# Optimization experiments

Measured on AMD Instinct MI355X. Metric: run time of the kernel, lower is better.

Reference implementation:

```python
import jax, jax.numpy as jnp
import numpy as np

N_GRAPHS = 500
CHAIN = 200
D_STATE = 64
HID = 128
NEG_SLOPE = 0.2  # PyG GATConv default


def setup_inputs() -> dict:
    key = jax.random.key(0)
    ks = jax.random.split(key, 9)
    N = N_GRAPHS * CHAIN
    # batched bidirectional chain graphs (as in create_chain_graph_batch)
    off = np.arange(N_GRAPHS, dtype=np.int32) * CHAIN
    a = (off[:, None] + np.arange(CHAIN - 1, dtype=np.int32)[None, :]).ravel()
    b = a + 1
    edge_index = jnp.asarray(np.stack([np.concatenate([a, b]), np.concatenate([b, a])]), dtype=jnp.int32)
    x = jax.random.normal(ks[0], (N, D_STATE), jnp.float32)
    s1 = 1.0 / np.sqrt(D_STATE)
    W1 = jax.random.normal(ks[1], (D_STATE, 2 * HID), jnp.float32) * s1
    att_src1 = jax.random.normal(ks[2], (2, HID), jnp.float32) * (1.0 / np.sqrt(HID))
    att_dst1 = jax.random.normal(ks[3], (2, HID), jnp.float32) * (1.0 / np.sqrt(HID))
    b1 = jnp.zeros((2 * HID,), jnp.float32)
    s2 = 1.0 / np.sqrt(2 * HID)
    W2 = jax.random.normal(ks[4], (2 * HID, HID), jnp.float32) * s2
    att_src2 = jax.random.normal(ks[5], (1, HID), jnp.float32) * (1.0 / np.sqrt(HID))
    att_dst2 = jax.random.normal(ks[6], (1, HID), jnp.float32) * (1.0 / np.sqrt(HID))
    b2 = jnp.zeros((HID,), jnp.float32)
    return {"x": x, "edge_index": edge_index, "W1": W1, "att_src1": att_src1,
            "att_dst1": att_dst1, "b1": b1, "W2": W2, "att_src2": att_src2,
            "att_dst2": att_dst2, "b2": b2}


def gat_conv(x, src, dst, W, att_src, att_dst, bias, concat):
    # PyG GATConv: per-head linear, additive attention, segment softmax over dst
    N = x.shape[0]
    H, C = att_src.shape
    h = (x @ W).reshape(N, H, C)                          # [N,H,C]
    a_s = (h * att_src).sum(-1)                           # [N,H]
    a_d = (h * att_dst).sum(-1)                           # [N,H]
    logits = jax.nn.leaky_relu(a_s[src] + a_d[dst], NEG_SLOPE)  # [E,H]
    m = jax.ops.segment_max(logits, dst, num_segments=N)
    e = jnp.exp(logits - m[dst])
    s = jax.ops.segment_sum(e, dst, num_segments=N)
    alpha = e / (s[dst] + 1e-16)                          # [E,H]
    out = jax.ops.segment_sum(h[src] * alpha[:, :, None], dst, num_segments=N)  # [N,H,C]
    out = out.reshape(N, H * C) if concat else out.mean(axis=1)
    return out + bias


def reference(x, edge_index, W1, att_src1, att_dst1, b1, W2, att_src2, att_dst2, b2):
    N = x.shape[0]
    loop = jnp.arange(N, dtype=edge_index.dtype)
    src = jnp.concatenate([edge_index[0], loop])  # add_self_loops=True (PyG default)
    dst = jnp.concatenate([edge_index[1], loop])
    h = gat_conv(x, src, dst, W1, att_src1, att_dst1, b1, concat=True)
    h = jax.nn.gelu(h, approximate=False)  # torch F.gelu default = exact erf
    h = gat_conv(h, src, dst, W2, att_src2, att_dst2, b2, concat=False)
    return jax.nn.gelu(h, approximate=False)
```

## Files before the change

kernel.cpp:

```cpp
#include <hip/hip_runtime.h>
#include <hip/hip_bf16.h>

#define NG 500
#define CH 200
#define NN (NG*CH)
#define DS 64
#define HDIM 128
#define C1 256
#define NEG_SLOPE 0.2f
#define GB 1563

typedef unsigned short ushort_t;
typedef __attribute__((ext_vector_type(8))) short bf16x8;
typedef __attribute__((ext_vector_type(4))) float f32x4;

__device__ __forceinline__ float us2f(ushort_t u){
  union { unsigned int i; float f; } v; v.i = ((unsigned int)u) << 16; return v.f;
}
__device__ __forceinline__ ushort_t f2us(float f){
  union { float f; unsigned int i; } v; v.f = f;
  unsigned int x = v.i;
  return (ushort_t)((x + 0x7fffu + ((x >> 16) & 1u)) >> 16);
}
__device__ __forceinline__ float lrelu(float v){ return v > 0.f ? v : NEG_SLOPE * v; }
__device__ __forceinline__ float gelu_fast(float x){
  float xc = fminf(fmaxf(x, -8.f), 8.f);
  float u  = 0.7978845608f * (xc + 0.044715f * xc * xc * xc);
  float e  = __expf(2.f * u);
  float t  = 1.f - 2.f / (e + 1.f);
  return 0.5f * x * (1.f + t);
}

__global__ void probe_dtype(const void* __restrict__ x, int* __restrict__ flag){
  __shared__ int cnt;
  if (threadIdx.x == 0) cnt = 0;
  __syncthreads();
  const ushort_t* p = (const ushort_t*)x;
  int local = 0;
  for (int i = threadIdx.x; i < 8192; i += 256) {
    float v = us2f(p[i]);
    if (!(fabsf(v) < 100.f)) local++;
  }
  atomicAdd(&cnt, local);
  __syncthreads();
  if (threadIdx.x == 0) flag[0] = (cnt > 16) ? 1 : 0;
}

__global__ void prep_w(const int* __restrict__ flag,
                       const void* W1, const void* as1, const void* ad1, const void* b1,
                       const void* W2, const void* as2, const void* ad2, const void* b2,
                       ushort_t* w1t, ushort_t* w2t,
                       float* asrc1f, float* adst1f, float* b1f,
                       float* asrc2f, float* adst2f, float* b2f)
{
  const bool F = flag[0] != 0;
  int i = blockIdx.x * 256 + threadIdx.x;
  #define LD(p, j) (F ? ((const float*)(p))[j] : us2f(((const ushort_t*)(p))[j]))
  if (i < 16384)      { int k = i >> 8, n = i & 255; w1t[n*64  + k] = f2us(LD(W1, i)); }
  else if (i < 49152) { int j = i - 16384, k = j >> 7, n = j & 127; w2t[n*256 + k] = f2us(LD(W2, j)); }
  else if (i < 49408) { asrc1f[i-49152] = LD(as1, i-49152); }
  else if (i < 49664) { adst1f[i-49408] = LD(ad1, i-49408); }
  else if (i < 49920) { b1f[i-49664]    = LD(b1,  i-49664); }
  else if (i < 50048) { asrc2f[i-49920] = LD(as2, i-49920); }
  else if (i < 50176) { adst2f[i-50048] = LD(ad2, i-50048); }
  else if (i < 50304) { b2f[i-50176]    = LD(b2,  i-50176); }
  #undef LD
}

__global__ __launch_bounds__(256, 3) void fused(
    const int* __restrict__ flag, const void* __restrict__ x,
    const ushort_t* __restrict__ w1t, const ushort_t* __restrict__ w2t,
    const float* __restrict__ asrc1f, const float* __restrict__ adst1f, const float* __restrict__ b1f,
    const float* __restrict__ asrc2f, const float* __restrict__ adst2f, const float* __restrict__ b2f,
    void* __restrict__ out)
{
  __shared__ ushort_t lds[22560];
  __shared__ float part_s[4][68], part_d[4][68];
  __shared__ float alp[66*8];
  ushort_t* As  = lds;
  ushort_t* Bs  = lds + 80*72;
  ushort_t* g1L = lds;
  ushort_t* Bs2 = lds + 68*264;

  const int t  = threadIdx.x;
  const int m0 = blockIdx.x * 64;
  const int l = t & 63, w = t >> 6;
  const int ln = l & 15, quad = l >> 4;
  const bool F = flag[0] != 0;

  #pragma unroll
  for (int i = 0; i < 5; i++) {
    int q = t + i*256;
    int r = q >> 4, off = (q & 15) * 4;
    int gr = m0 - 2 + r;
    ushort4 v = {0,0,0,0};
    if (r < 68 && gr >= 0 && gr < NN) {
      if (F) {
        float4 xv = *(const float4*)(&((const float*)x)[(size_t)gr*DS + off]);
        v.x = f2us(xv.x); v.y = f2us(xv.y); v.z = f2us(xv.z); v.w = f2us(xv.w);
      } else {
        v = *(const ushort4*)(&((const ushort_t*)x)[(size_t)gr*DS + off]);
      }
    }
    *(ushort4*)(&As[r*72 + off]) = v;
  }

  f32x4 acc[5][4];
  #pragma unroll
  for (int mi = 0; mi < 5; mi++)
    #pragma unroll
    for (int nj = 0; nj < 4; nj++) acc[mi][nj] = (f32x4){0.f,0.f,0.f,0.f};

  #pragma unroll
  for (int h = 0; h < 2; h++) {
    #pragma unroll
    for (int i = 0; i < 4; i++) {
      int u = t + i*256;
      int rl = u >> 3, off = (u & 7) * 8;
      int wv = rl >> 5, rem = rl & 31;
      int grow = wv*64 + h*32 + rem;
      *(uint4*)(&Bs[rl*72 + off]) = *(const uint4*)(&w1t[grow*64 + off]);
    }
    __syncthreads();
    #pragma unroll
    for (int ks = 0; ks < 2; ks++) {
      const int kk = ks*32 + quad*8;
      bf16x8 a[5], b[2];
      #pragma unroll
      for (int mi = 0; mi < 5; mi++) a[mi] = *(const bf16x8*)(&As[(mi*16 + ln)*72 + kk]);
      #pragma unroll
      for (int njl = 0; njl < 2; njl++) b[njl] = *(const bf16x8*)(&Bs[(w*32 + njl*16 + ln)*72 + kk]);
      #pragma unroll
      for (int mi = 0; mi < 5; mi++)
        #pragma unroll
        for (int njl = 0; njl < 2; njl++)
          acc[mi][2*h+njl] = __builtin_amdgcn_mfma_f32_16x16x32_bf16(a[mi], b[njl], acc[mi][2*h+njl], 0, 0, 0);
    }
    __syncthreads();
  }

  {
    float wsv[4], wdv[4];
    #pragma unroll
    for (int nj = 0; nj < 4; nj++) {
      wsv[nj] = asrc1f[w*64 + nj*16 + ln];
      wdv[nj] = adst1f[w*64 + nj*16 + ln];
    }
    #pragma unroll
    for (int mi = 0; mi < 5; mi++)
      #pragma unroll
      for (int r = 0; r < 4; r++) {
        float s = 0.f, d = 0.f;
        #pragma unroll
        for (int nj = 0; nj < 4; nj++) { s += acc[mi][nj][r] * wsv[nj]; d += acc[mi][nj][r] * wdv[nj]; }
        #pragma unroll
        for (int o = 1; o < 16; o <<= 1) { s += __shfl_xor(s, o, 64); d += __shfl_xor(d, o, 64); }
        int row = mi*16 + quad*4 + r;
        if (ln == 0 && row < 68) { part_s[w][row] = s; part_d[w][row] = d; }
      }
  }
  __syncthreads();

  if (t < 132) {
    int hh = (t >= 66) ? 1 : 0;
    int n  = t - 66*hh;
    int gj = m0 - 1 + n;
    int p  = gj % CH;
    float ad   = part_d[2*hh][n+1] + part_d[2*hh+1][n+1];
    float as_s = part_s[2*hh][n+1] + part_s[2*hh+1][n+1];
    float as_l = part_s[2*hh][n  ] + part_s[2*hh+1][n  ];
    float as_r = part_s[2*hh][n+2] + part_s[2*hh+1][n+2];
    bool hl = p > 0, hr = p < CH-1;
    float zs = lrelu(as_s + ad);
    float zl = hl ? lrelu(as_l + ad) : -1e30f;
    float zr = hr ? lrelu(as_r + ad) : -1e30f;
    float mx = fmaxf(zs, fmaxf(zl, zr));
    float el = hl ? __expf(zl - mx) : 0.f;
    float es = __expf(zs - mx);
    float er = hr ? __expf(zr - mx) : 0.f;
    float inv = 1.f / (el + es + er + 1e-16f);
    alp[n*8 + hh*4 + 0] = el*inv; alp[n*8 + hh*4 + 1] = es*inv; alp[n*8 + hh*4 + 2] = er*inv;
  }
  __syncthreads();

  {
    float b1v[4];
    #pragma unroll
    for (int nj = 0; nj < 4; nj++) b1v[nj] = b1f[w*64 + nj*16 + ln];
    if (t < 132) {
      int rr = (t < 66) ? 0 : 67;
      int c4 = ((t < 66) ? t : t - 66) * 4;
      ushort4 z = {0,0,0,0};
      *(ushort4*)(&g1L[rr*264 + c4]) = z;
    }
    const int head = w >> 1;
    #pragma unroll
    for (int mi = 0; mi < 5; mi++) {
      const int mip = (mi < 4) ? mi+1 : 4;
      const int mim = (mi > 0) ? mi-1 : 0;
      float hp3[4], hm0[4];
      #pragma unroll
      for (int nj = 0; nj < 4; nj++) {
        float up_a = __shfl(acc[mi ][nj][0], (l+16)&63, 64);
        float up_b = __shfl(acc[mip][nj][0], (l+16)&63, 64);
        float dn_a = __shfl(acc[mi ][nj][3], (l-16)&63, 64);
        float dn_b = __shfl(acc[mim][nj][3], (l-16)&63, 64);
        hp3[nj] = (quad < 3) ? up_a : up_b;
        hm0[nj] = (quad > 0) ? dn_a : dn_b;
      }
      #pragma unroll
      for (int r = 0; r < 4; r++) {
        int row = mi*16 + quad*4 + r;
        if (row >= 1 && row <= 66) {
          float4 av = *(const float4*)(&alp[(row-1)*8 + head*4]);
          #pragma unroll
          for (int nj = 0; nj < 4; nj++) {
            float self = acc[mi][nj][r];
            float hm = (r > 0) ? acc[mi][nj][r-1] : hm0[nj];
            float hp = (r < 3) ? acc[mi][nj][r+1] : hp3[nj];
            float v = av.y*self + av.x*hm + av.z*hp + b1v[nj];
            g1L[row*264 + w*64 + nj*16 + ln] = f2us(gelu_fast(v));
          }
        }
      }
    }
  }
  __syncthreads();

  f32x4 acc2[5][2];
  #pragma unroll
  for (int mi = 0; mi < 5; mi++)
    #pragma unroll
    for (int nj = 0; nj < 2; nj++) acc2[mi][nj] = (f32x4){0.f,0.f,0.f,0.f};

  #pragma unroll
  for (int ck = 0; ck < 4; ck++) {
    bf16x8 a2[2][5];
    #pragma unroll
    for (int ks = 0; ks < 2; ks++)
      #pragma unroll
      for (int mi = 0; mi < 5; mi++) {
        int ar = mi*16 + ln;
        if (mi == 4) ar = (ar < 67) ? ar : 67;
        a2[ks][mi] = *(const bf16x8*)(&g1L[ar*264 + ck*64 + ks*32 + quad*8]);
      }
    #pragma unroll
    for (int h2 = 0; h2 < 2; h2++) {
      #pragma unroll
      for (int i = 0; i < 2; i++) {
        int u = t + i*256;
        int rl = u >> 3, off = (u & 7) * 8;
        int wv = rl >> 4, j = rl & 15;
        int grow = wv*32 + h2*16 + j;
        *(uint4*)(&Bs2[rl*72 + off]) = *(const uint4*)(&w2t[grow*256 + ck*64 + off]);
      }
      __syncthreads();
      #pragma unroll
      for (int ks = 0; ks < 2; ks++) {
        bf16x8 b = *(const bf16x8*)(&Bs2[(w*16 + ln)*72 + ks*32 + quad*8]);
        #pragma unroll
        for (int mi = 0; mi < 5; mi++)
          acc2[mi][h2] = __builtin_amdgcn_mfma_f32_16x16x32_bf16(a2[ks][mi], b, acc2[mi][h2], 0, 0, 0);
      }
      __syncthreads();
    }
  }

  {
    float ws2[2], wd2[2];
    #pragma unroll
    for (int nj = 0; nj < 2; nj++) {
      ws2[nj] = asrc2f[w*32 + nj*16 + ln];
      wd2[nj] = adst2f[w*32 + nj*16 + ln];
    }
    #pragma unroll
    for (int mi = 0; mi < 5; mi++)
      #pragma unroll
      for (int r = 0; r < 4; r++) {
        float s = 0.f, d = 0.f;
        #pragma unroll
        for (int nj = 0; nj < 2; nj++) { s += acc2[mi][nj][r] * ws2[nj]; d += acc2[mi][nj][r] * wd2[nj]; }
        #pragma unroll
        for (int o = 1; o < 16; o <<= 1) { s += __shfl_xor(s, o, 64); d += __shfl_xor(d, o, 64); }
        int row = mi*16 + quad*4 + r;
        if (ln == 0 && row < 68) { part_s[w][row] = s; part_d[w][row] = d; }
      }
  }
  __syncthreads();

  if (t < 64) {
    int gi = m0 + t;
    if (gi < NN) {
      int p = gi % CH;
      float ad = 0.f, as_s = 0.f, as_l = 0.f, as_r = 0.f;
      #pragma unroll
      for (int ww = 0; ww < 4; ww++) {
        ad   += part_d[ww][t+2];
        as_s += part_s[ww][t+2];
        as_l += part_s[ww][t+1];
        as_r += part_s[ww][t+3];
      }
      bool hl = p > 0, hr = p < CH-1;
      float zs = lrelu(as_s + ad);
      float zl = hl ? lrelu(as_l + ad) : -1e30f;
      float zr = hr ? lrelu(as_r + ad) : -1e30f;
      float mx = fmaxf(zs, fmaxf(zl, zr));
      float el = hl ? __expf(zl - mx) : 0.f;
      float es = __expf(zs - mx);
      float er = hr ? __expf(zr - mx) : 0.f;
      float inv = 1.f / (el + es + er + 1e-16f);
      alp[t*4 + 0] = el*inv; alp[t*4 + 1] = es*inv; alp[t*4 + 2] = er*inv;
    }
  }
  __syncthreads();

  {
    float b2v[2];
    #pragma unroll
    for (int nj = 0; nj < 2; nj++) b2v[nj] = b2f[w*32 + nj*16 + ln];
    #pragma unroll
    for (int mi = 0; mi < 5; mi++) {
      const int mip = (mi < 4) ? mi+1 : 4;
      const int mim = (mi > 0) ? mi-1 : 0;
      float hp3[2], hm0[2];
      #pragma unroll
      for (int nj = 0; nj < 2; nj++) {
        float up_a = __shfl(acc2[mi ][nj][0], (l+16)&63, 64);
        float up_b = __shfl(acc2[mip][nj][0], (l+16)&63, 64);
        float dn_a = __shfl(acc2[mi ][nj][3], (l-16)&63, 64);
        float dn_b = __shfl(acc2[mim][nj][3], (l-16)&63, 64);
        hp3[nj] = (quad < 3) ? up_a : up_b;
        hm0[nj] = (quad > 0) ? dn_a : dn_b;
      }
      #pragma unroll
      for (int r = 0; r < 4; r++) {
        int row = mi*16 + quad*4 + r;
        if (row >= 2 && row <= 65) {
          int n = row - 2;
          int gi = m0 + n;
          if (gi < NN) {
            float4 av = *(const float4*)(&alp[n*4]);
            #pragma unroll
            for (int nj = 0; nj < 2; nj++) {
              float self = acc2[mi][nj][r];
              float hm = (r > 0) ? acc2[mi][nj][r-1] : hm0[nj];
              float hp = (r < 3) ? acc2[mi][nj][r+1] : hp3[nj];
              float v = av.y*self + av.x*hm + av.z*hp + b2v[nj];
              float o = gelu_fast(v);
              int c2 = w*32 + nj*16 + ln;
              if (F) ((float*)out)[(size_t)gi*HDIM + c2] = o;
              else   ((ushort_t*)out)[(size_t)gi*HDIM + c2] = f2us(o);
            }
          }
        }
      }
    }
  }
}

extern "C" void kernel_launch(void* const* d_in, const int* in_sizes, int n_in,
                              void* d_out, int out_size, void* d_ws, size_t ws_size,
                              hipStream_t stream)
{
  const void* x   = d_in[0];
  const void* W1  = d_in[2];
  const void* as1 = d_in[3];
  const void* ad1 = d_in[4];
  const void* b1  = d_in[5];
  const void* W2  = d_in[6];
  const void* as2 = d_in[7];
  const void* ad2 = d_in[8];
  const void* b2  = d_in[9];

  char* w = (char*)d_ws;
  size_t off = 0;
  int* flag = (int*)w;                       off += 256;
  ushort_t* w1t = (ushort_t*)(w + off);      off += 64 * 256 * 2;
  ushort_t* w2t = (ushort_t*)(w + off);      off += 256 * 128 * 2;
  float* asrc1f = (float*)(w + off);         off += 256 * 4;
  float* adst1f = (float*)(w + off);         off += 256 * 4;
  float* b1f    = (float*)(w + off);         off += 256 * 4;
  float* asrc2f = (float*)(w + off);         off += 128 * 4;
  float* adst2f = (float*)(w + off);         off += 128 * 4;
  float* b2f    = (float*)(w + off);         off += 128 * 4;

  probe_dtype<<<1, 256, 0, stream>>>(x, flag);
  prep_w<<<197, 256, 0, stream>>>(flag, W1, as1, ad1, b1, W2, as2, ad2, b2,
                                  w1t, w2t, asrc1f, adst1f, b1f, asrc2f, adst2f, b2f);
  fused<<<GB, 256, 0, stream>>>(flag, x, w1t, w2t, asrc1f, adst1f, b1f,
                                asrc2f, adst2f, b2f, d_out);
}
```

Baseline: 189.4 us.

## Load GEMM weight fragments directly from global memory and raise occupancy

The W1 and W2 tiles are no longer staged through shared memory. Each wave now reads its bf16 B fragments straight from global memory (served by L2/L1 cache), which removes the staging stores and most per-chunk barriers. The LDS array shrinks, and the launch bound is raised to 4 blocks per CU so more blocks can be resident. GELU is also replaced by a sigmoid-form tanh approximation without clamping. The trade-offs are uncoalesced, per-lane global reads for the weights, higher register pressure under the tighter occupancy bound, and slightly different GELU numerics.

```diff
diff --git a/kernel.cpp b/kernel.cpp
--- a/kernel.cpp
+++ b/kernel.cpp
@@ -24,11 +24,10 @@
 }
 __device__ __forceinline__ float lrelu(float v){ return v > 0.f ? v : NEG_SLOPE * v; }
 __device__ __forceinline__ float gelu_fast(float x){
-  float xc = fminf(fmaxf(x, -8.f), 8.f);
-  float u  = 0.7978845608f * (xc + 0.044715f * xc * xc * xc);
-  float e  = __expf(2.f * u);
-  float t  = 1.f - 2.f / (e + 1.f);
-  return 0.5f * x * (1.f + t);
+  float x2 = x * x;
+  float z  = x * fmaf(0.0713548162726f, x2, 1.59576912161f);
+  float e  = __expf(-z);
+  return x / fmaf(e, 1.f, 1.f) ;
 }
 
 __global__ void probe_dtype(const void* __restrict__ x, int* __restrict__ flag){
@@ -67,20 +66,18 @@
   #undef LD
 }
 
-__global__ __launch_bounds__(256, 3) void fused(
+__global__ __launch_bounds__(256, 4) void fused(
     const int* __restrict__ flag, const void* __restrict__ x,
     const ushort_t* __restrict__ w1t, const ushort_t* __restrict__ w2t,
     const float* __restrict__ asrc1f, const float* __restrict__ adst1f, const float* __restrict__ b1f,
     const float* __restrict__ asrc2f, const float* __restrict__ adst2f, const float* __restrict__ b2f,
     void* __restrict__ out)
 {
-  __shared__ ushort_t lds[22560];
+  __shared__ ushort_t lds[17952];
   __shared__ float part_s[4][68], part_d[4][68];
   __shared__ float alp[66*8];
   ushort_t* As  = lds;
-  ushort_t* Bs  = lds + 80*72;
   ushort_t* g1L = lds;
-  ushort_t* Bs2 = lds + 68*264;
 
   const int t  = threadIdx.x;
   const int m0 = blockIdx.x * 64;
@@ -111,32 +108,24 @@
     #pragma unroll
     for (int nj = 0; nj < 4; nj++) acc[mi][nj] = (f32x4){0.f,0.f,0.f,0.f};
 
+  __syncthreads();
   #pragma unroll
   for (int h = 0; h < 2; h++) {
-    #pragma unroll
-    for (int i = 0; i < 4; i++) {
-      int u = t + i*256;
-      int rl = u >> 3, off = (u & 7) * 8;
-      int wv = rl >> 5, rem = rl & 31;
-      int grow = wv*64 + h*32 + rem;
-      *(uint4*)(&Bs[rl*72 + off]) = *(const uint4*)(&w1t[grow*64 + off]);
-    }
-    __syncthreads();
     #pragma unroll
     for (int ks = 0; ks < 2; ks++) {
       const int kk = ks*32 + quad*8;
       bf16x8 a[5], b[2];
       #pragma unroll
+      for (int njl = 0; njl < 2; njl++)
+        b[njl] = *(const bf16x8*)(&w1t[(w*64 + h*32 + njl*16 + ln)*64 + kk]);
+      #pragma unroll
       for (int mi = 0; mi < 5; mi++) a[mi] = *(const bf16x8*)(&As[(mi*16 + ln)*72 + kk]);
-      #pragma unroll
-      for (int njl = 0; njl < 2; njl++) b[njl] = *(const bf16x8*)(&Bs[(w*32 + njl*16 + ln)*72 + kk]);
       #pragma unroll
       for (int mi = 0; mi < 5; mi++)
         #pragma unroll
         for (int njl = 0; njl < 2; njl++)
           acc[mi][2*h+njl] = __builtin_amdgcn_mfma_f32_16x16x32_bf16(a[mi], b[njl], acc[mi][2*h+njl], 0, 0, 0);
     }
-    __syncthreads();
   }
 
   {
@@ -247,22 +236,12 @@
     #pragma unroll
     for (int h2 = 0; h2 < 2; h2++) {
       #pragma unroll
-      for (int i = 0; i < 2; i++) {
-        int u = t + i*256;
-        int rl = u >> 3, off = (u & 7) * 8;
-        int wv = rl >> 4, j = rl & 15;
-        int grow = wv*32 + h2*16 + j;
-        *(uint4*)(&Bs2[rl*72 + off]) = *(const uint4*)(&w2t[grow*256 + ck*64 + off]);
-      }
-      __syncthreads();
-      #pragma unroll
       for (int ks = 0; ks < 2; ks++) {
-        bf16x8 b = *(const bf16x8*)(&Bs2[(w*16 + ln)*72 + ks*32 + quad*8]);
+        bf16x8 b = *(const bf16x8*)(&w2t[(w*32 + h2*16 + ln)*256 + ck*64 + ks*32 + quad*8]);
         #pragma unroll
         for (int mi = 0; mi < 5; mi++)
           acc2[mi][h2] = __builtin_amdgcn_mfma_f32_16x16x32_bf16(a2[ks][mi], b, acc2[mi][h2], 0, 0, 0);
       }
-      __syncthreads();
     }
   }
 
```

Result: faster. 173.6 us (-8.4%).
